# Performance work log

Measured on AMD Instinct MI355X. Metric: run time of the kernel, lower is better.

## Reference

```python
import jax, jax.numpy as jnp
import numpy as np

NEG_SLOPE = 0.2

def gat_conv(x, edge_index, W, a_src, a_dst, bias, heads, channels):
    # PyG GATConv (add_self_loops=False, dropout off in eval)
    N = x.shape[0]
    h = (x @ W).reshape(N, heads, channels)               # [N,H,C]
    src, dst = edge_index[0], edge_index[1]
    e_src = jnp.einsum('nhc,hc->nh', h, a_src)            # [N,H]
    e_dst = jnp.einsum('nhc,hc->nh', h, a_dst)
    e = jax.nn.leaky_relu(e_src[src] + e_dst[dst], NEG_SLOPE)  # [E,H]
    # softmax over incoming edges of each destination node
    m = jax.ops.segment_max(e, dst, num_segments=N)       # [N,H]
    ex = jnp.exp(e - m[dst])
    s = jax.ops.segment_sum(ex, dst, num_segments=N)
    alpha = ex / (s[dst] + 1e-16)                         # [E,H]
    msg = h[src] * alpha[:, :, None]                      # [E,H,C]
    out = jax.ops.segment_sum(msg, dst, num_segments=N)   # [N,H,C]
    return out.reshape(N, heads * channels) + bias


def setup_inputs() -> dict:
    key = jax.random.key(0)
    ks = jax.random.split(key, 12)
    N, E, SED, HID, H, F_OUT = 20000, 320000, 768, 128, 4, 128
    return {
        'x': jax.random.normal(ks[0], (N, SED), jnp.float32),
        'edge_index': jax.random.randint(ks[1], (2, E), 0, N, jnp.int32),
        'sentence_embedding': jax.random.normal(ks[2], (SED,), jnp.float32),
        'W1': jax.random.normal(ks[3], (2 * SED, H * HID), jnp.float32) * 0.02,
        'a1_src': jax.random.normal(ks[4], (H, HID), jnp.float32) * 0.1,
        'a1_dst': jax.random.normal(ks[5], (H, HID), jnp.float32) * 0.1,
        'b1': jax.random.normal(ks[6], (H * HID,), jnp.float32) * 0.02,
        'W2': jax.random.normal(ks[7], (H * HID, F_OUT), jnp.float32) * 0.02,
        'a2_src': jax.random.normal(ks[8], (1, F_OUT), jnp.float32) * 0.1,
        'a2_dst': jax.random.normal(ks[9], (1, F_OUT), jnp.float32) * 0.1,
        'b2': jax.random.normal(ks[10], (F_OUT,), jnp.float32) * 0.02,
    }


def reference(x, edge_index, sentence_embedding, W1, a1_src, a1_dst, b1, W2, a2_src, a2_dst, b2):
    N = x.shape[0]
    sent = jnp.broadcast_to(sentence_embedding[None, :], (N, sentence_embedding.shape[0]))
    h = jnp.concatenate([x, sent], axis=1)                # [N, 2*SED]
    h = gat_conv(h, edge_index, W1, a1_src, a1_dst, b1, heads=4, channels=128)
    h = jax.nn.elu(h)
    out = gat_conv(h, edge_index, W2, a2_src, a2_dst, b2, heads=1, channels=128)
    return out
```

## Files before the change

### kernel.cpp

```cpp
#include <hip/hip_runtime.h>
#include <cstdint>
#include <cstddef>

#define NSLOPE 0.2f

typedef __attribute__((ext_vector_type(8))) short bf16x8;
typedef __attribute__((ext_vector_type(4))) float f32x4;
typedef __attribute__((ext_vector_type(2))) float f32x2;
typedef unsigned short ushort_t;

__device__ inline ushort_t f2bf(float f) {
    union { float f; unsigned u; } v; v.f = f;
    unsigned u = v.u;
    unsigned r = (u + 0x7fffu + ((u >> 16) & 1u)) >> 16;
    return (ushort_t)r;
}
__device__ inline float bf2f(ushort_t u) {
    union { unsigned u; float f; } v; v.u = ((unsigned)u) << 16;
    return v.f;
}
__device__ inline float2 unpack_bf2(unsigned u) {
    return make_float2(bf2f((ushort_t)(u & 0xffffu)), bf2f((ushort_t)(u >> 16)));
}
__device__ inline f32x2 unpack2(unsigned u) {
    union { unsigned u; float f; } lo, hi;
    lo.u = u << 16;
    hi.u = u & 0xffff0000u;
    f32x2 r; r.x = lo.f; r.y = hi.f;
    return r;
}
__device__ inline float leaky(float v) { return (v > 0.f) ? v : NSLOPE * v; }
__device__ inline float sel4(float4 q, bool b1, bool b2) {
    return b2 ? (b1 ? q.w : q.z) : (b1 ? q.y : q.x);
}

__global__ __launch_bounds__(256) void prep_kernel(
    const float* __restrict__ x, ushort_t* __restrict__ x_bf16, size_t nx,
    const float* __restrict__ W1, ushort_t* __restrict__ W1T,
    const float* __restrict__ W2, ushort_t* __restrict__ W2T,
    const float* __restrict__ sent, float* __restrict__ svec_part,
    int* __restrict__ indeg, int N, int nbCast, int nbZero)
{
    __shared__ float tile[32][33];
    int bid = blockIdx.x;
    int tid = threadIdx.x;
    if (bid < nbCast) {
        size_t i = ((size_t)bid * 256 + tid) * 8;
        if (i < nx) {
            float4 v0 = *(const float4*)(x + i);
            float4 v1 = *(const float4*)(x + i + 4);
            ushort_t r[8] = { f2bf(v0.x), f2bf(v0.y), f2bf(v0.z), f2bf(v0.w),
                              f2bf(v1.x), f2bf(v1.y), f2bf(v1.z), f2bf(v1.w) };
            *(uint4*)(x_bf16 + i) = *(uint4*)r;
        }
        return;
    }
    bid -= nbCast;
    if (bid < 384) {
        int k0 = (bid % 24) * 32, n0 = (bid / 24) * 32;
        int tx = tid & 31, ty = tid >> 5;
#pragma unroll
        for (int i = 0; i < 4; ++i)
            tile[ty + i * 8][tx] = W1[(size_t)(k0 + ty + i * 8) * 512 + n0 + tx];
        __syncthreads();
#pragma unroll
        for (int i = 0; i < 4; ++i)
            W1T[(size_t)(n0 + ty + i * 8) * 768 + k0 + tx] = f2bf(tile[tx][ty + i * 8]);
        return;
    }
    bid -= 384;
    if (bid < 64) {
        int k0 = (bid % 16) * 32, n0 = (bid / 16) * 32;
        int tx = tid & 31, ty = tid >> 5;
#pragma unroll
        for (int i = 0; i < 4; ++i)
            tile[ty + i * 8][tx] = W2[(size_t)(k0 + ty + i * 8) * 128 + n0 + tx];
        __syncthreads();
#pragma unroll
        for (int i = 0; i < 4; ++i)
            W2T[(size_t)(n0 + ty + i * 8) * 512 + k0 + tx] = f2bf(tile[tx][ty + i * 8]);
        return;
    }
    bid -= 64;
    if (bid < 16) {
        int cb = bid & 1, kb = bid >> 1;
        int c = cb * 256 + tid;
        int k0 = kb * 96;
        float acc = 0.f;
#pragma unroll 8
        for (int k = k0; k < k0 + 96; ++k)
            acc += sent[k] * W1[(size_t)(768 + k) * 512 + c];
        svec_part[kb * 512 + c] = acc;
        return;
    }
    bid -= 16;
    {
        int i = bid * 256 + tid;
        if (i < N) indeg[i] = 0;
    }
}

__device__ inline void async_copy16(const void* g, void* l) {
    __builtin_amdgcn_global_load_lds(
        (const __attribute__((address_space(1))) unsigned int*)g,
        (__attribute__((address_space(3))) unsigned int*)l, 16, 0, 0);
}

__global__ __launch_bounds__(256) void mfma_gemm_kernel(
    const ushort_t* __restrict__ A,
    const ushort_t* __restrict__ BT,
    const float* __restrict__ bias,
    ushort_t* __restrict__ Cb,
    const float* __restrict__ asrc,
    const float* __restrict__ adst,
    float* __restrict__ e_src,
    float* __restrict__ e_dst,
    int eStride,
    int M, int K, int Nc)
{
    __shared__ __align__(16) ushort_t lA[128 * 32];
    __shared__ __align__(16) ushort_t lB[128 * 32];
    __shared__ float e_lds[128][2][2];
    const int tid = threadIdx.x;
    const int wave = tid >> 6;
    const int lane = tid & 63;
    const int row0 = blockIdx.x * 128;
    const int col0 = blockIdx.y * 128;
    const int wm = (wave & 1) * 64;
    const int wn = (wave >> 1) * 64;
    const int q = lane >> 4;
    const int ml = lane & 15;

    f32x4 acc[4][4] = {};

    int rowS[2], gS[2];
#pragma unroll
    for (int i = 0; i < 2; ++i) {
        int p = wave * 128 + i * 64 + lane;
        int r = p >> 2, s = p & 3;
        rowS[i] = r;
        gS[i] = s ^ ((r >> 1) & 3);
    }

    for (int k0 = 0; k0 < K; k0 += 32) {
#pragma unroll
        for (int i = 0; i < 2; ++i) {
            int pb = wave * 128 + i * 64;
            int r = rowS[i];
            int ga = min(row0 + r, M - 1);
            async_copy16(A + (size_t)ga * K + k0 + gS[i] * 8, &lA[(size_t)pb * 8]);
            async_copy16(BT + (size_t)(col0 + r) * K + k0 + gS[i] * 8, &lB[(size_t)pb * 8]);
        }
        __syncthreads();
        bf16x8 af[4], bfr[4];
#pragma unroll
        for (int t = 0; t < 4; ++t) {
            int m = wm + t * 16 + ml;
            af[t] = *(const bf16x8*)&lA[(size_t)(m * 4 + (q ^ ((m >> 1) & 3))) * 8];
            int n = wn + t * 16 + ml;
            bfr[t] = *(const bf16x8*)&lB[(size_t)(n * 4 + (q ^ ((n >> 1) & 3))) * 8];
        }
#pragma unroll
        for (int tm = 0; tm < 4; ++tm)
#pragma unroll
            for (int tn = 0; tn < 4; ++tn)
                acc[tm][tn] = __builtin_amdgcn_mfma_f32_16x16x32_bf16(
                    af[tm], bfr[tn], acc[tm][tn], 0, 0, 0);
        __syncthreads();
    }

    float es_acc[4][4] = {};
    float ed_acc[4][4] = {};
#pragma unroll
    for (int tm = 0; tm < 4; ++tm) {
        int rbase = row0 + wm + tm * 16 + q * 4;
#pragma unroll
        for (int tn = 0; tn < 4; ++tn) {
            int col = col0 + wn + tn * 16 + ml;
            float bb = bias ? bias[col] : 0.f;
            float av = asrc[col];
            float dv = adst[col];
#pragma unroll
            for (int r = 0; r < 4; ++r) {
                int row = rbase + r;
                float val = acc[tm][tn][r] + bb;
                if (row < M)
                    Cb[(size_t)row * Nc + col] = f2bf(val);
                es_acc[tm][r] += val * av;
                ed_acc[tm][r] += val * dv;
            }
        }
    }
    const int colhalf = wave >> 1;
#pragma unroll
    for (int tm = 0; tm < 4; ++tm) {
#pragma unroll
        for (int r = 0; r < 4; ++r) {
            float es = es_acc[tm][r], ed2 = ed_acc[tm][r];
#pragma unroll
            for (int st = 1; st < 16; st <<= 1) {
                es += __shfl_xor(es, st);
                ed2 += __shfl_xor(ed2, st);
            }
            if (ml == 0) {
                int rl = wm + tm * 16 + q * 4 + r;
                e_lds[rl][colhalf][0] = es;
                e_lds[rl][colhalf][1] = ed2;
            }
        }
    }
    __syncthreads();
    if (tid < 128) {
        int row = row0 + tid;
        if (row < M) {
            float es = e_lds[tid][0][0] + e_lds[tid][1][0];
            float ed2 = e_lds[tid][0][1] + e_lds[tid][1][1];
            e_src[(size_t)row * eStride + blockIdx.y] = es;
            e_dst[(size_t)row * eStride + blockIdx.y] = ed2;
        }
    }
}

__global__ void count_kernel(const int* __restrict__ ei, int* __restrict__ indeg, int E) {
    int e = blockIdx.x * blockDim.x + threadIdx.x;
    if (e < E) atomicAdd(&indeg[ei[E + e]], 1);
}

__global__ __launch_bounds__(1024) void scan_kernel(const int* __restrict__ indeg,
                                                    int* __restrict__ offsets,
                                                    int* __restrict__ cursor,
                                                    const float* __restrict__ svec_part,
                                                    float* __restrict__ svec, int N) {
    __shared__ int partial[1024];
    int tid = threadIdx.x;
    if (tid < 512) {
        float s = 0.f;
#pragma unroll
        for (int kb = 0; kb < 8; ++kb) s += svec_part[kb * 512 + tid];
        svec[tid] = s;
    }
    int per = (N + 1023) / 1024;
    int start = tid * per;
    int end = min(start + per, N);
    int sum = 0;
    if (start + per <= N && (per & 3) == 0) {
        for (int i = 0; i < per; i += 4) {
            int4 v = *(const int4*)(indeg + start + i);
            sum += v.x + v.y + v.z + v.w;
        }
    } else {
        for (int i = start; i < end; ++i) sum += indeg[i];
    }
    partial[tid] = sum;
    __syncthreads();
    for (int st = 1; st < 1024; st <<= 1) {
        int v = (tid >= st) ? partial[tid - st] : 0;
        __syncthreads();
        partial[tid] += v;
        __syncthreads();
    }
    int run = (tid == 0) ? 0 : partial[tid - 1];
    if (start + per <= N && (per & 3) == 0) {
        for (int i = 0; i < per; i += 4) {
            int4 v = *(const int4*)(indeg + start + i);
            int4 o;
            o.x = run;
            o.y = o.x + v.x;
            o.z = o.y + v.y;
            o.w = o.z + v.z;
            run = o.w + v.w;
            *(int4*)(offsets + start + i) = o;
            *(int4*)(cursor + start + i) = o;
        }
    } else {
        for (int i = start; i < end; ++i) {
            offsets[i] = run; cursor[i] = run;
            run += indeg[i];
        }
    }
    if (tid == 1023) offsets[N] = run;
}

__global__ void scatter_kernel(const int* __restrict__ ei, int* __restrict__ cursor,
                               int* __restrict__ csr_src, int E) {
    int e = blockIdx.x * blockDim.x + threadIdx.x;
    if (e < E) {
        int d = ei[E + e];
        int p = atomicAdd(&cursor[d], 1);
        csr_src[p] = ei[e];
    }
}

__global__ __launch_bounds__(256) void gather1_kernel(
    const ushort_t* __restrict__ h1b, const float* __restrict__ e_src,
    const float* __restrict__ e_dst, const int* __restrict__ offsets,
    const int* __restrict__ csr_src, const float* __restrict__ bias,
    ushort_t* __restrict__ outb, int N)
{
    int node = __builtin_amdgcn_readfirstlane(blockIdx.x * 4 + (threadIdx.x >> 6));
    int lane = threadIdx.x & 63;
    if (node >= N) return;
    int beg = offsets[node], end = offsets[node + 1];
    float4 ed = *(const float4*)&e_dst[node * 4];

    float m[4] = { -1e30f, -1e30f, -1e30f, -1e30f };
    float s[4] = { 0.f, 0.f, 0.f, 0.f };
    for (int j = beg + lane; j < end; j += 64) {
        int sid = csr_src[j];
        float4 es = *(const float4*)&e_src[sid * 4];
        float e[4] = { leaky(es.x + ed.x), leaky(es.y + ed.y),
                       leaky(es.z + ed.z), leaky(es.w + ed.w) };
#pragma unroll
        for (int hh = 0; hh < 4; ++hh) {
            float nm = fmaxf(m[hh], e[hh]);
            s[hh] = s[hh] * __expf(m[hh] - nm) + __expf(e[hh] - nm);
            m[hh] = nm;
        }
    }
#pragma unroll
    for (int st = 32; st >= 1; st >>= 1) {
#pragma unroll
        for (int hh = 0; hh < 4; ++hh) {
            float om = __shfl_xor(m[hh], st);
            float os = __shfl_xor(s[hh], st);
            float nm = fmaxf(m[hh], om);
            s[hh] = s[hh] * __expf(m[hh] - nm) + os * __expf(om - nm);
            m[hh] = nm;
        }
    }
    const int h = lane >> 4;
    const bool b1 = (h & 1), b2 = (h & 2);
    float mh  = b2 ? (b1 ? m[3] : m[2]) : (b1 ? m[1] : m[0]);
    float sh  = b2 ? (b1 ? s[3] : s[2]) : (b1 ? s[1] : s[0]);
    float rsh = 1.f / (sh + 1e-16f);
    float edh = sel4(ed, b1, b2);

    const ushort_t* hp = h1b + lane * 8;
    f32x2 acc[4] = {};
    int j = beg;
#pragma unroll 2
    for (; j + 4 <= end; j += 4) {
        int s0 = csr_src[j], s1 = csr_src[j + 1];
        int s2 = csr_src[j + 2], s3 = csr_src[j + 3];
        float4 q0 = *(const float4*)&e_src[s0 * 4];
        float4 q1 = *(const float4*)&e_src[s1 * 4];
        float4 q2 = *(const float4*)&e_src[s2 * 4];
        float4 q3 = *(const float4*)&e_src[s3 * 4];
        float w0 = __expf(leaky(sel4(q0, b1, b2) + edh) - mh) * rsh;
        float w1 = __expf(leaky(sel4(q1, b1, b2) + edh) - mh) * rsh;
        float w2 = __expf(leaky(sel4(q2, b1, b2) + edh) - mh) * rsh;
        float w3 = __expf(leaky(sel4(q3, b1, b2) + edh) - mh) * rsh;
        uint4 u0 = *(const uint4*)&hp[(size_t)s0 * 512];
        uint4 u1 = *(const uint4*)&hp[(size_t)s1 * 512];
        uint4 u2 = *(const uint4*)&hp[(size_t)s2 * 512];
        uint4 u3 = *(const uint4*)&hp[(size_t)s3 * 512];
        f32x2 wv;
        wv.x = w0; wv.y = w0;
        acc[0] += unpack2(u0.x) * wv; acc[1] += unpack2(u0.y) * wv;
        acc[2] += unpack2(u0.z) * wv; acc[3] += unpack2(u0.w) * wv;
        wv.x = w1; wv.y = w1;
        acc[0] += unpack2(u1.x) * wv; acc[1] += unpack2(u1.y) * wv;
        acc[2] += unpack2(u1.z) * wv; acc[3] += unpack2(u1.w) * wv;
        wv.x = w2; wv.y = w2;
        acc[0] += unpack2(u2.x) * wv; acc[1] += unpack2(u2.y) * wv;
        acc[2] += unpack2(u2.z) * wv; acc[3] += unpack2(u2.w) * wv;
        wv.x = w3; wv.y = w3;
        acc[0] += unpack2(u3.x) * wv; acc[1] += unpack2(u3.y) * wv;
        acc[2] += unpack2(u3.z) * wv; acc[3] += unpack2(u3.w) * wv;
    }
    for (; j < end; ++j) {
        int s0 = csr_src[j];
        float4 q0 = *(const float4*)&e_src[s0 * 4];
        float w0 = __expf(leaky(sel4(q0, b1, b2) + edh) - mh) * rsh;
        uint4 u0 = *(const uint4*)&hp[(size_t)s0 * 512];
        f32x2 wv; wv.x = w0; wv.y = w0;
        acc[0] += unpack2(u0.x) * wv; acc[1] += unpack2(u0.y) * wv;
        acc[2] += unpack2(u0.z) * wv; acc[3] += unpack2(u0.w) * wv;
    }
    int c = lane * 8;
    ushort_t o[8];
#pragma unroll
    for (int i = 0; i < 4; ++i) {
        float r0 = acc[i].x + bias[c + 2 * i];
        float r1 = acc[i].y + bias[c + 2 * i + 1];
        r0 = (r0 > 0.f) ? r0 : (__expf(r0) - 1.f);
        r1 = (r1 > 0.f) ? r1 : (__expf(r1) - 1.f);
        o[2 * i] = f2bf(r0);
        o[2 * i + 1] = f2bf(r1);
    }
    *(uint4*)&outb[(size_t)node * 512 + c] = *(uint4*)o;
}

__global__ __launch_bounds__(256) void gather2_kernel(
    const ushort_t* __restrict__ h2b, const float* __restrict__ e_src,
    const float* __restrict__ e_dst, const int* __restrict__ offsets,
    const int* __restrict__ csr_src, const float* __restrict__ bias,
    float* __restrict__ out, int N)
{
    int node = __builtin_amdgcn_readfirstlane(blockIdx.x * 4 + (threadIdx.x >> 6));
    int lane = threadIdx.x & 63;
    if (node >= N) return;
    int beg = offsets[node], end = offsets[node + 1];
    float ed = e_dst[node];

    float m = -1e30f, s = 0.f;
    for (int j = beg + lane; j < end; j += 64) {
        float e = leaky(e_src[csr_src[j]] + ed);
        float nm = fmaxf(m, e);
        s = s * __expf(m - nm) + __expf(e - nm);
        m = nm;
    }
#pragma unroll
    for (int st = 32; st >= 1; st >>= 1) {
        float om = __shfl_xor(m, st);
        float os = __shfl_xor(s, st);
        float nm = fmaxf(m, om);
        s = s * __expf(m - nm) + os * __expf(om - nm);
        m = nm;
    }
    float rs = 1.f / (s + 1e-16f);

    const ushort_t* hp = h2b + lane * 2;
    f32x2 acc = { 0.f, 0.f };
    int j = beg;
#pragma unroll 2
    for (; j + 4 <= end; j += 4) {
        int s0 = csr_src[j], s1 = csr_src[j + 1];
        int s2 = csr_src[j + 2], s3 = csr_src[j + 3];
        float w0 = __expf(leaky(e_src[s0] + ed) - m) * rs;
        float w1 = __expf(leaky(e_src[s1] + ed) - m) * rs;
        float w2 = __expf(leaky(e_src[s2] + ed) - m) * rs;
        float w3 = __expf(leaky(e_src[s3] + ed) - m) * rs;
        unsigned u0 = *(const unsigned*)&hp[(size_t)s0 * 128];
        unsigned u1 = *(const unsigned*)&hp[(size_t)s1 * 128];
        unsigned u2 = *(const unsigned*)&hp[(size_t)s2 * 128];
        unsigned u3 = *(const unsigned*)&hp[(size_t)s3 * 128];
        f32x2 w0v = { w0, w0 }, w1v = { w1, w1 }, w2v = { w2, w2 }, w3v = { w3, w3 };
        acc += unpack2(u0) * w0v;
        acc += unpack2(u1) * w1v;
        acc += unpack2(u2) * w2v;
        acc += unpack2(u3) * w3v;
    }
    for (; j < end; ++j) {
        int s0 = csr_src[j];
        float w0 = __expf(leaky(e_src[s0] + ed) - m) * rs;
        unsigned u0 = *(const unsigned*)&hp[(size_t)s0 * 128];
        f32x2 w0v = { w0, w0 };
        acc += unpack2(u0) * w0v;
    }
    float2 o = make_float2(acc.x + bias[lane * 2], acc.y + bias[lane * 2 + 1]);
    *(float2*)&out[(size_t)node * 128 + lane * 2] = o;
}

extern "C" void kernel_launch(void* const* d_in, const int* in_sizes, int n_in,
                              void* d_out, int out_size, void* d_ws, size_t ws_size,
                              hipStream_t stream) {
    const float* x      = (const float*)d_in[0];
    const int*   ei     = (const int*)  d_in[1];
    const float* sent   = (const float*)d_in[2];
    const float* W1     = (const float*)d_in[3];
    const float* a1_src = (const float*)d_in[4];
    const float* a1_dst = (const float*)d_in[5];
    const float* b1     = (const float*)d_in[6];
    const float* W2     = (const float*)d_in[7];
    const float* a2_src = (const float*)d_in[8];
    const float* a2_dst = (const float*)d_in[9];
    const float* b2     = (const float*)d_in[10];
    float* out = (float*)d_out;

    const int N = in_sizes[0] / 768;
    const int E = in_sizes[1] / 2;

    char* p = (char*)d_ws;
    auto carve = [&](size_t bytes) {
        char* q = p;
        p += (bytes + 255) & ~(size_t)255;
        return q;
    };
    ushort_t* h1b = (ushort_t*)carve((size_t)N * 512 * 2);
    char* shared_region = carve((size_t)N * 768 * 2);
    ushort_t* x_bf16 = (ushort_t*)shared_region;
    ushort_t* h_elu_b = (ushort_t*)shared_region;
    ushort_t* h2b = (ushort_t*)carve((size_t)N * 128 * 2);
    ushort_t* W1T = (ushort_t*)carve((size_t)512 * 768 * 2);
    ushort_t* W2T = (ushort_t*)carve((size_t)128 * 512 * 2);
    float* svec_part = (float*)carve(8 * 512 * 4);
    float* svec   = (float*)carve(512 * 4);
    float* e_src1 = (float*)carve((size_t)N * 4 * 4);
    float* e_dst1 = (float*)carve((size_t)N * 4 * 4);
    float* e_src2 = (float*)carve((size_t)N * 4);
    float* e_dst2 = (float*)carve((size_t)N * 4);
    int*   indeg  = (int*)carve((size_t)N * 4);
    int*   offs   = (int*)carve((size_t)(N + 1) * 4);
    int*   cursor = (int*)carve((size_t)N * 4);
    int*   csrsrc = (int*)carve((size_t)E * 4);

    size_t nx = (size_t)N * 768;
    int nbCast = (int)((nx / 8 + 255) / 256);
    int nbZero = (N + 255) / 256;
    int nbPrep = nbCast + 384 + 64 + 16 + nbZero;

    prep_kernel<<<nbPrep, 256, 0, stream>>>(x, x_bf16, nx, W1, W1T, W2, W2T,
                                            sent, svec_part, indeg, N, nbCast, nbZero);
    count_kernel<<<(E + 255) / 256, 256, 0, stream>>>(ei, indeg, E);
    scan_kernel<<<1, 1024, 0, stream>>>(indeg, offs, cursor, svec_part, svec, N);
    scatter_kernel<<<(E + 255) / 256, 256, 0, stream>>>(ei, cursor, csrsrc, E);

    mfma_gemm_kernel<<<dim3((N + 127) / 128, 4), 256, 0, stream>>>(
        x_bf16, W1T, svec, h1b, a1_src, a1_dst, e_src1, e_dst1, 4, N, 768, 512);

    gather1_kernel<<<(N + 3) / 4, 256, 0, stream>>>(
        h1b, e_src1, e_dst1, offs, csrsrc, b1, h_elu_b, N);

    mfma_gemm_kernel<<<dim3((N + 127) / 128, 1), 256, 0, stream>>>(
        h_elu_b, W2T, nullptr, h2b, a2_src, a2_dst, e_src2, e_dst2, 1, N, 512, 128);

    gather2_kernel<<<(N + 3) / 4, 256, 0, stream>>>(
        h2b, e_src2, e_dst2, offs, csrsrc, b2, out, N);
}
```

Measured before the change: 295.4 us.

## Double-buffer LDS tiles in MFMA GEMM and swap grid order for A reuse

The GEMM kernel now keeps two LDS buffers for the A and B tiles. It issues the async global-to-LDS copy for the next K slice before running the MFMAs on the current slice, so loads overlap compute. This also drops one barrier per iteration. The grid is transposed so column blocks vary fastest, letting blocks that share the same A rows run close together and reuse A from L2. The cost is double the LDS per block, which may lower occupancy.

```diff
diff --git a/kernel.cpp b/kernel.cpp
--- a/kernel.cpp
+++ b/kernel.cpp
@@ -118,14 +118,14 @@
     int eStride,
     int M, int K, int Nc)
 {
-    __shared__ __align__(16) ushort_t lA[128 * 32];
-    __shared__ __align__(16) ushort_t lB[128 * 32];
+    __shared__ __align__(16) ushort_t lA[2][128 * 32];
+    __shared__ __align__(16) ushort_t lB[2][128 * 32];
     __shared__ float e_lds[128][2][2];
     const int tid = threadIdx.x;
     const int wave = tid >> 6;
     const int lane = tid & 63;
-    const int row0 = blockIdx.x * 128;
-    const int col0 = blockIdx.y * 128;
+    const int col0 = blockIdx.x * 128;
+    const int row0 = blockIdx.y * 128;
     const int wm = (wave & 1) * 64;
     const int wn = (wave >> 1) * 64;
     const int q = lane >> 4;
@@ -142,23 +142,29 @@
         gS[i] = s ^ ((r >> 1) & 3);
     }
 
-    for (int k0 = 0; k0 < K; k0 += 32) {
+    auto stage = [&](int k0, int buf) {
 #pragma unroll
         for (int i = 0; i < 2; ++i) {
             int pb = wave * 128 + i * 64;
             int r = rowS[i];
             int ga = min(row0 + r, M - 1);
-            async_copy16(A + (size_t)ga * K + k0 + gS[i] * 8, &lA[(size_t)pb * 8]);
-            async_copy16(BT + (size_t)(col0 + r) * K + k0 + gS[i] * 8, &lB[(size_t)pb * 8]);
-        }
-        __syncthreads();
+            async_copy16(A + (size_t)ga * K + k0 + gS[i] * 8, &lA[buf][(size_t)pb * 8]);
+            async_copy16(BT + (size_t)(col0 + r) * K + k0 + gS[i] * 8, &lB[buf][(size_t)pb * 8]);
+        }
+    };
+
+    stage(0, 0);
+    __syncthreads();
+    int pb = 0;
+    for (int k0 = 0; k0 < K; k0 += 32) {
+        if (k0 + 32 < K) stage(k0 + 32, pb ^ 1);
         bf16x8 af[4], bfr[4];
 #pragma unroll
         for (int t = 0; t < 4; ++t) {
             int m = wm + t * 16 + ml;
-            af[t] = *(const bf16x8*)&lA[(size_t)(m * 4 + (q ^ ((m >> 1) & 3))) * 8];
+            af[t] = *(const bf16x8*)&lA[pb][(size_t)(m * 4 + (q ^ ((m >> 1) & 3))) * 8];
             int n = wn + t * 16 + ml;
-            bfr[t] = *(const bf16x8*)&lB[(size_t)(n * 4 + (q ^ ((n >> 1) & 3))) * 8];
+            bfr[t] = *(const bf16x8*)&lB[pb][(size_t)(n * 4 + (q ^ ((n >> 1) & 3))) * 8];
         }
 #pragma unroll
         for (int tm = 0; tm < 4; ++tm)
@@ -167,6 +173,7 @@
                 acc[tm][tn] = __builtin_amdgcn_mfma_f32_16x16x32_bf16(
                     af[tm], bfr[tn], acc[tm][tn], 0, 0, 0);
         __syncthreads();
+        pb ^= 1;
     }
 
     float es_acc[4][4] = {};
@@ -215,8 +222,8 @@
         if (row < M) {
             float es = e_lds[tid][0][0] + e_lds[tid][1][0];
             float ed2 = e_lds[tid][0][1] + e_lds[tid][1][1];
-            e_src[(size_t)row * eStride + blockIdx.y] = es;
-            e_dst[(size_t)row * eStride + blockIdx.y] = ed2;
+            e_src[(size_t)row * eStride + blockIdx.x] = es;
+            e_dst[(size_t)row * eStride + blockIdx.x] = ed2;
         }
     }
 }
@@ -506,13 +513,13 @@
     scan_kernel<<<1, 1024, 0, stream>>>(indeg, offs, cursor, svec_part, svec, N);
     scatter_kernel<<<(E + 255) / 256, 256, 0, stream>>>(ei, cursor, csrsrc, E);
 
-    mfma_gemm_kernel<<<dim3((N + 127) / 128, 4), 256, 0, stream>>>(
+    mfma_gemm_kernel<<<dim3(4, (N + 127) / 128), 256, 0, stream>>>(
         x_bf16, W1T, svec, h1b, a1_src, a1_dst, e_src1, e_dst1, 4, N, 768, 512);
 
     gather1_kernel<<<(N + 3) / 4, 256, 0, stream>>>(
         h1b, e_src1, e_dst1, offs, csrsrc, b1, h_elu_b, N);
 
-    mfma_gemm_kernel<<<dim3((N + 127) / 128, 1), 256, 0, stream>>>(
+    mfma_gemm_kernel<<<dim3(1, (N + 127) / 128), 256, 0, stream>>>(
         h_elu_b, W2T, nullptr, h2b, a2_src, a2_dst, e_src2, e_dst2, 1, N, 512, 128);
 
     gather2_kernel<<<(N + 3) / 4, 256, 0, stream>>>(
```

Result: no change. 295.2 us (-0.1%).
